# Kernel optimization log

Hardware: AMD Instinct MI355X
Metric: run time of the kernel (lower is better)

## Reference

```python
import math
import jax, jax.numpy as jnp
import numpy as np

N, C, T, V = 32, 64, 256, 25
EPS = 1e-5


def setup_inputs() -> dict:
    key = jax.random.key(0)
    ks = jax.random.split(key, 4)
    # kaiming fan_out init scale for 1x1 conv: std = sqrt(2 / C_out)
    std = math.sqrt(2.0 / C)
    return {
        "x": jax.random.normal(ks[0], (N, C, T, V), dtype=jnp.float32),
        "Wq": jax.random.normal(ks[1], (C, C), dtype=jnp.float32) * std,
        "bq": jnp.zeros((C,), dtype=jnp.float32),
        "Wk": jax.random.normal(ks[2], (C, C), dtype=jnp.float32) * std,
        "bk": jnp.zeros((C,), dtype=jnp.float32),
        "Wv": jax.random.normal(ks[3], (C, C), dtype=jnp.float32) * std,
        "bv": jnp.zeros((C,), dtype=jnp.float32),
        "gamma": jnp.ones((C,), dtype=jnp.float32),
        "beta": jnp.zeros((C,), dtype=jnp.float32),
    }


def _proj(x, W, b):
    # 1x1 conv over [N, Cin, T, V] then permute(0,3,2,1) -> [N, V, T, Cout]
    return jnp.einsum('nctv,dc->nvtd', x, W) + b


def reference(x, Wq, bq, Wk, bk, Wv, bv, gamma, beta):
    c_out = Wq.shape[0]
    q = _proj(x, Wq, bq)                                  # [N,V,T,C]
    k = _proj(x, Wk, bk)                                  # [N,V,T,C]
    v = _proj(x, Wv, bv)                                  # [N,V,T,C]
    att = jnp.einsum('nvsc,nvtc->nvst', q, k) / math.sqrt(c_out)
    att = jnp.tanh(att)                                   # [N,V,T,T]
    out = jnp.einsum('nvst,nvtc->nvsc', att, v)           # [N,V,T,C]
    out = jnp.transpose(out, (0, 3, 2, 1))                # [N,C,T,V]
    # BatchNorm2d, training mode (batch stats, biased variance)
    mean = jnp.mean(out, axis=(0, 2, 3), keepdims=True)
    var = jnp.var(out, axis=(0, 2, 3), keepdims=True)
    g = gamma[None, :, None, None]
    b = beta[None, :, None, None]
    return (out - mean) * jax.lax.rsqrt(var + EPS) * g + b
```

## Files before the change

### kernel.cpp

```cpp
#include <hip/hip_runtime.h>
#include <hip/hip_bf16.h>
#include <math.h>

#define NN 32
#define CC 64
#define TT 256
#define VV 25
#define PAD 68
#define RS (VV * CC)
#define PERN (TT * VV * CC)

#define KST 72
#define VST 40
#define PST 40
#define XST 72
#define FST 68

typedef __attribute__((ext_vector_type(8))) short bf16x8;
typedef __attribute__((ext_vector_type(4))) float f32x4;

__device__ __forceinline__ float fast_tanh(float x) {
  float ax = fabsf(x);
  float e = __expf(-2.0f * ax);
  float r = 1.0f - 2.0f * e / (1.0f + e);
  return copysignf(r, x);
}
__device__ __forceinline__ unsigned short f2bf(float f) {
  unsigned u = __float_as_uint(f);
  u += 0x7fff + ((u >> 16) & 1u);
  return (unsigned short)(u >> 16);
}
__device__ __forceinline__ float bf2f(unsigned short h) {
  return __uint_as_float(((unsigned)h) << 16);
}
__device__ __forceinline__ void cvt8(float4 a, float4 b, bf16x8& h8, bf16x8& l8) {
  unsigned short h;
  h = f2bf(a.x); h8[0] = (short)h; l8[0] = (short)f2bf(a.x - bf2f(h));
  h = f2bf(a.y); h8[1] = (short)h; l8[1] = (short)f2bf(a.y - bf2f(h));
  h = f2bf(a.z); h8[2] = (short)h; l8[2] = (short)f2bf(a.z - bf2f(h));
  h = f2bf(a.w); h8[3] = (short)h; l8[3] = (short)f2bf(a.w - bf2f(h));
  h = f2bf(b.x); h8[4] = (short)h; l8[4] = (short)f2bf(b.x - bf2f(h));
  h = f2bf(b.y); h8[5] = (short)h; l8[5] = (short)f2bf(b.y - bf2f(h));
  h = f2bf(b.z); h8[6] = (short)h; l8[6] = (short)f2bf(b.z - bf2f(h));
  h = f2bf(b.w); h8[7] = (short)h; l8[7] = (short)f2bf(b.w - bf2f(h));
}

__global__ void k0_zero(float* __restrict__ p) { p[threadIdx.x] = 0.0f; }

__global__ void k_wsplit(const float* __restrict__ Wq, const float* __restrict__ Wk,
                         const float* __restrict__ Wv, const float* __restrict__ bq,
                         const float* __restrict__ bk, const float* __restrict__ bv,
                         unsigned short* __restrict__ wh, unsigned short* __restrict__ wl,
                         float* __restrict__ bcat, float* __restrict__ stats)
{
  const int tid = threadIdx.x;
  if (tid < 128) stats[tid] = 0.0f;
  for (int i = 0; i < 48; ++i) {
    int idx = i * 256 + tid;
    int r = idx >> 6, c = idx & 63;
    int m = r >> 6, ch = r & 63;
    const float* W = (m == 0) ? Wq : (m == 1) ? Wk : Wv;
    float w = W[ch * 64 + c];
    unsigned short h = f2bf(w);
    wh[idx] = h;
    wl[idx] = f2bf(w - bf2f(h));
  }
  if (tid < 192) {
    int m = tid >> 6, ch = tid & 63;
    const float* B = (m == 0) ? bq : (m == 1) ? bk : bv;
    bcat[tid] = B[ch];
  }
}

__global__ __launch_bounds__(256, 2)
void k_proj_mfma(const float* __restrict__ x,
                 const unsigned short* __restrict__ wh,
                 const unsigned short* __restrict__ wl,
                 const float* __restrict__ bcat,
                 float* __restrict__ qb, float* __restrict__ kb,
                 float* __restrict__ vb)
{
  __shared__ short Xbuf[2 * 128 * XST];
  short* Xh = Xbuf;
  short* Xl = Xbuf + 128 * XST;

  const int tid  = threadIdx.x;
  const int lane = tid & 63;
  const int wid  = tid >> 6;
  const int l15  = lane & 15;
  const int g    = lane >> 4;
  const int band = wid * 48;

  const int n = blockIdx.x / 50;
  const int chunk = blockIdx.x - n * 50;
  const int tv0 = chunk * 128;
  const float* xn = x + (size_t)n * PERN + tv0;

  {
    const int cg  = tid >> 5;
    const int tvl = (tid & 31) * 4;
    #pragma unroll
    for (int r = 0; r < 2; ++r) {
      const int c0 = r * 32 + cg * 4;
      float4 r0 = *(const float4*)&xn[(size_t)(c0 + 0) * (TT * VV) + tvl];
      float4 r1 = *(const float4*)&xn[(size_t)(c0 + 1) * (TT * VV) + tvl];
      float4 r2 = *(const float4*)&xn[(size_t)(c0 + 2) * (TT * VV) + tvl];
      float4 r3 = *(const float4*)&xn[(size_t)(c0 + 3) * (TT * VV) + tvl];
      #pragma unroll
      for (int j = 0; j < 4; ++j) {
        float v0 = (&r0.x)[j], v1 = (&r1.x)[j], v2 = (&r2.x)[j], v3 = (&r3.x)[j];
        unsigned short h0 = f2bf(v0), h1 = f2bf(v1), h2 = f2bf(v2), h3 = f2bf(v3);
        *(short4*)&Xh[(tvl + j) * XST + c0] =
            make_short4((short)h0, (short)h1, (short)h2, (short)h3);
        *(short4*)&Xl[(tvl + j) * XST + c0] =
            make_short4((short)f2bf(v0 - bf2f(h0)), (short)f2bf(v1 - bf2f(h1)),
                        (short)f2bf(v2 - bf2f(h2)), (short)f2bf(v3 - bf2f(h3)));
      }
    }
  }

  bf16x8 wfh[3][2], wfl[3][2];
  #pragma unroll
  for (int rt = 0; rt < 3; ++rt)
    #pragma unroll
    for (int ks = 0; ks < 2; ++ks) {
      size_t off = (size_t)(band + rt * 16 + l15) * 64 + ks * 32 + g * 8;
      wfh[rt][ks] = *(const bf16x8*)&wh[off];
      wfl[rt][ks] = *(const bf16x8*)&wl[off];
    }
  float bc[3][4];
  #pragma unroll
  for (int rt = 0; rt < 3; ++rt)
    #pragma unroll
    for (int r = 0; r < 4; ++r)
      bc[rt][r] = bcat[band + rt * 16 + 4 * g + r];

  __syncthreads();

  f32x4 acc[3][8];
  #pragma unroll
  for (int rt = 0; rt < 3; ++rt)
    #pragma unroll
    for (int ct = 0; ct < 8; ++ct)
      acc[rt][ct] = (f32x4){0.f, 0.f, 0.f, 0.f};

  #pragma unroll
  for (int ct = 0; ct < 8; ++ct) {
    bf16x8 xh[2], xl[2];
    #pragma unroll
    for (int ks = 0; ks < 2; ++ks) {
      xh[ks] = *(const bf16x8*)&Xh[(ct * 16 + l15) * XST + ks * 32 + g * 8];
      xl[ks] = *(const bf16x8*)&Xl[(ct * 16 + l15) * XST + ks * 32 + g * 8];
    }
    #pragma unroll
    for (int rt = 0; rt < 3; ++rt)
      #pragma unroll
      for (int ks = 0; ks < 2; ++ks) {
        acc[rt][ct] = __builtin_amdgcn_mfma_f32_16x16x32_bf16(wfh[rt][ks], xh[ks], acc[rt][ct], 0, 0, 0);
        acc[rt][ct] = __builtin_amdgcn_mfma_f32_16x16x32_bf16(wfh[rt][ks], xl[ks], acc[rt][ct], 0, 0, 0);
        acc[rt][ct] = __builtin_amdgcn_mfma_f32_16x16x32_bf16(wfl[rt][ks], xh[ks], acc[rt][ct], 0, 0, 0);
      }
  }

  #pragma unroll
  for (int rt = 0; rt < 3; ++rt)
    #pragma unroll
    for (int ct = 0; ct < 8; ++ct)
      #pragma unroll
      for (int r = 0; r < 4; ++r)
        acc[rt][ct][r] += bc[rt][r];

  float* Fbuf = (float*)Xbuf;
  #pragma unroll
  for (int m = 0; m < 3; ++m) {
    __syncthreads();
    #pragma unroll
    for (int rt = 0; rt < 3; ++rt) {
      int grow = band + rt * 16;
      if ((grow >> 6) == m) {
        int ch = (grow & 63) + 4 * g;
        #pragma unroll
        for (int ct = 0; ct < 8; ++ct)
          *(f32x4*)&Fbuf[(ct * 16 + l15) * FST + ch] = acc[rt][ct];
      }
    }
    __syncthreads();
    float* gd = (m == 0 ? qb : m == 1 ? kb : vb) + (size_t)n * PERN + (size_t)tv0 * CC;
    #pragma unroll
    for (int i = 0; i < 8; ++i) {
      int e = i * 256 + tid;
      int tv = e >> 4, c4 = (e & 15) * 4;
      *(float4*)&gd[(size_t)e * 4] = *(const float4*)&Fbuf[tv * FST + c4];
    }
  }
}

__global__ __launch_bounds__(256, 2)
void k_attn_mfma(const float* __restrict__ qb, const float* __restrict__ kb,
                 const float* __restrict__ vb, float* __restrict__ stats,
                 float* __restrict__ ob)
{
  __shared__ short KhL[2][32 * KST], KlL[2][32 * KST];
  __shared__ short VhL[2][64 * VST], VlL[2][64 * VST];
  __shared__ short Pwh[4][64 * PST], Pwl[4][64 * PST];
  __shared__ float red1[256], red2[256];

  const int tid  = threadIdx.x;
  const int lane = tid & 63;
  const int wid  = tid >> 6;
  const int l15  = lane & 15;
  const int g    = lane >> 4;
  const int band = wid * 64;
  const int bid  = blockIdx.x;
  const int n = bid / VV, v = bid - n * VV;
  const size_t base = (size_t)n * PERN + (size_t)v * CC;

  const int sr = tid >> 3;
  const int sc = (tid & 7) * 8;

  bf16x8 qh[4][2], ql[4][2];
  #pragma unroll
  for (int rt = 0; rt < 4; ++rt) {
    #pragma unroll
    for (int ks = 0; ks < 2; ++ks) {
      const float* p = qb + base + (size_t)(band + rt * 16 + l15) * RS + ks * 32 + g * 8;
      cvt8(*(const float4*)p, *(const float4*)(p + 4), qh[rt][ks], ql[rt][ks]);
    }
  }

  f32x4 acc[4][4];
  #pragma unroll
  for (int i = 0; i < 4; ++i)
    #pragma unroll
    for (int j = 0; j < 4; ++j)
      acc[i][j] = (f32x4){0.f, 0.f, 0.f, 0.f};

  {
    const float* kp = kb + base + (size_t)sr * RS + sc;
    const float* vp = vb + base + (size_t)sr * RS + sc;
    float4 ka = *(const float4*)kp, kb4 = *(const float4*)(kp + 4);
    float4 va = *(const float4*)vp, vb4 = *(const float4*)(vp + 4);
    bf16x8 h8, l8;
    cvt8(ka, kb4, h8, l8);
    *(bf16x8*)&KhL[0][sr * KST + sc] = h8;
    *(bf16x8*)&KlL[0][sr * KST + sc] = l8;
    cvt8(va, vb4, h8, l8);
    #pragma unroll
    for (int j = 0; j < 8; ++j) {
      VhL[0][(sc + j) * VST + sr] = h8[j];
      VlL[0][(sc + j) * VST + sr] = l8[j];
    }
  }

  int cur = 0;
  for (int tl = 0; tl < 8; ++tl) {
    __syncthreads();
    const bool more = (tl < 7);
    float4 ka, kb4, va, vb4;
    if (more) {
      const float* kp = kb + base + (size_t)((tl + 1) * 32 + sr) * RS + sc;
      const float* vp = vb + base + (size_t)((tl + 1) * 32 + sr) * RS + sc;
      ka = *(const float4*)kp; kb4 = *(const float4*)(kp + 4);
      va = *(const float4*)vp; vb4 = *(const float4*)(vp + 4);
    }

    bf16x8 kfh[2][2], kfl[2][2];
    #pragma unroll
    for (int ct = 0; ct < 2; ++ct)
      #pragma unroll
      for (int ks = 0; ks < 2; ++ks) {
        kfh[ct][ks] = *(const bf16x8*)&KhL[cur][(ct * 16 + l15) * KST + ks * 32 + g * 8];
        kfl[ct][ks] = *(const bf16x8*)&KlL[cur][(ct * 16 + l15) * KST + ks * 32 + g * 8];
      }
    #pragma unroll
    for (int rt = 0; rt < 4; ++rt) {
      #pragma unroll
      for (int ct = 0; ct < 2; ++ct) {
        f32x4 s = (f32x4){0.f, 0.f, 0.f, 0.f};
        #pragma unroll
        for (int ks = 0; ks < 2; ++ks) {
          s = __builtin_amdgcn_mfma_f32_16x16x32_bf16(qh[rt][ks], kfh[ct][ks], s, 0, 0, 0);
          s = __builtin_amdgcn_mfma_f32_16x16x32_bf16(qh[rt][ks], kfl[ct][ks], s, 0, 0, 0);
          s = __builtin_amdgcn_mfma_f32_16x16x32_bf16(ql[rt][ks], kfh[ct][ks], s, 0, 0, 0);
        }
        #pragma unroll
        for (int r = 0; r < 4; ++r) {
          float p = fast_tanh(s[r] * 0.125f);
          unsigned short h = f2bf(p);
          int row = rt * 16 + 4 * g + r;
          Pwh[wid][row * PST + ct * 16 + l15] = (short)h;
          Pwl[wid][row * PST + ct * 16 + l15] = (short)f2bf(p - bf2f(h));
        }
      }
    }

    bf16x8 vfh[4], vfl[4], pfh[4], pfl[4];
    #pragma unroll
    for (int i = 0; i < 4; ++i) {
      vfh[i] = *(const bf16x8*)&VhL[cur][(i * 16 + l15) * VST + g * 8];
      vfl[i] = *(const bf16x8*)&VlL[cur][(i * 16 + l15) * VST + g * 8];
      pfh[i] = *(const bf16x8*)&Pwh[wid][(i * 16 + l15) * PST + g * 8];
      pfl[i] = *(const bf16x8*)&Pwl[wid][(i * 16 + l15) * PST + g * 8];
    }
    #pragma unroll
    for (int ctc = 0; ctc < 4; ++ctc) {
      #pragma unroll
      for (int st = 0; st < 4; ++st) {
        acc[ctc][st] = __builtin_amdgcn_mfma_f32_16x16x32_bf16(vfh[ctc], pfh[st], acc[ctc][st], 0, 0, 0);
        acc[ctc][st] = __builtin_amdgcn_mfma_f32_16x16x32_bf16(vfh[ctc], pfl[st], acc[ctc][st], 0, 0, 0);
        acc[ctc][st] = __builtin_amdgcn_mfma_f32_16x16x32_bf16(vfl[ctc], pfh[st], acc[ctc][st], 0, 0, 0);
      }
    }

    if (more) {
      int nb = cur ^ 1;
      bf16x8 h8, l8;
      cvt8(ka, kb4, h8, l8);
      *(bf16x8*)&KhL[nb][sr * KST + sc] = h8;
      *(bf16x8*)&KlL[nb][sr * KST + sc] = l8;
      cvt8(va, vb4, h8, l8);
      #pragma unroll
      for (int j = 0; j < 8; ++j) {
        VhL[nb][(sc + j) * VST + sr] = h8[j];
        VlL[nb][(sc + j) * VST + sr] = l8[j];
      }
    }
    cur ^= 1;
  }

  #pragma unroll
  for (int ctc = 0; ctc < 4; ++ctc) {
    #pragma unroll
    for (int r = 0; r < 4; ++r) {
      float s1 = 0.f, s2 = 0.f;
      #pragma unroll
      for (int st = 0; st < 4; ++st) { float vv = acc[ctc][st][r]; s1 += vv; s2 += vv * vv; }
      #pragma unroll
      for (int m = 1; m <= 8; m <<= 1) {
        s1 += __shfl_xor(s1, m, 64);
        s2 += __shfl_xor(s2, m, 64);
      }
      if (l15 == 0) {
        int c = ctc * 16 + 4 * g + r;
        red1[wid * 64 + c] = s1;
        red2[wid * 64 + c] = s2;
      }
    }
  }
  __syncthreads();
  if (tid < 64) {
    float a1 = red1[tid] + red1[64 + tid] + red1[128 + tid] + red1[192 + tid];
    float a2 = red2[tid] + red2[64 + tid] + red2[128 + tid] + red2[192 + tid];
    atomicAdd(&stats[tid], a1);
    atomicAdd(&stats[64 + tid], a2);
  }

  float* obp = ob + base;
  #pragma unroll
  for (int st = 0; st < 4; ++st)
    #pragma unroll
    for (int ctc = 0; ctc < 4; ++ctc)
      *(f32x4*)&obp[(size_t)(band + st * 16 + l15) * RS + ctc * 16 + 4 * g] = acc[ctc][st];
}

__global__ void k2_stats(const float* __restrict__ stats,
                         const float* __restrict__ gamma,
                         const float* __restrict__ beta,
                         float* __restrict__ ss)
{
  int c = threadIdx.x;
  if (c < 64) {
    const float M = (float)(NN * TT * VV);
    float mean = stats[c] / M;
    float var = stats[64 + c] / M - mean * mean;
    float sc = gamma[c] * rsqrtf(var + 1e-5f);
    ss[c] = sc;
    ss[64 + c] = beta[c] - mean * sc;
  }
}

__global__ __launch_bounds__(256)
void k3_emit(const float* __restrict__ ob, const float* __restrict__ ss,
             float* __restrict__ out)
{
  __shared__ float tile[VV * 8 * 65];
  __shared__ float scl[64], sft[64];
  const int bid = blockIdx.x;
  const int n = bid >> 5, sb = bid & 31;
  const int tid = threadIdx.x;
  if (tid < 64) { scl[tid] = ss[tid]; sft[tid] = ss[64 + tid]; }
  const float* src = ob + (size_t)n * PERN + (size_t)sb * 8 * RS;
  #pragma unroll
  for (int i = 0; i < 25; ++i) {
    int e2 = i * 512 + tid * 2;
    float2 f = *(const float2*)&src[e2];
    int c = e2 & 63;
    int r = e2 >> 6;
    int tL = r / 25, vv2 = r - tL * 25;
    tile[(vv2 * 8 + tL) * 65 + c] = f.x;
    tile[(vv2 * 8 + tL) * 65 + c + 1] = f.y;
  }
  __syncthreads();
  float* outn = out + (size_t)n * CC * TT * VV + sb * 8 * VV;
  for (int e = tid; e < CC * 200; e += 256) {
    int c = e / 200, r = e - c * 200;
    int tL = r / 25, v = r - tL * 25;
    float val = tile[(v * 8 + tL) * 65 + c];
    outn[(size_t)c * TT * VV + tL * VV + v] = val * scl[c] + sft[c];
  }
}

__global__ void k3b_inplace(float* __restrict__ out, const float* __restrict__ ss) {
  __shared__ float scl[64], sft[64];
  if (threadIdx.x < 64) { scl[threadIdx.x] = ss[threadIdx.x]; sft[threadIdx.x] = ss[64 + threadIdx.x]; }
  __syncthreads();
  const size_t total = (size_t)NN * CC * TT * VV;
  size_t i = ((size_t)blockIdx.x * 256 + threadIdx.x) * 4;
  const size_t stride = (size_t)gridDim.x * 256 * 4;
  for (; i < total; i += stride) {
    float4 val = *(float4*)(out + i);
    int c = (int)((i / (TT * VV)) & 63);
    val.x = val.x * scl[c] + sft[c];
    val.y = val.y * scl[c] + sft[c];
    val.z = val.z * scl[c] + sft[c];
    val.w = val.w * scl[c] + sft[c];
    *(float4*)(out + i) = val;
  }
}

__device__ __forceinline__ void proj_row(const float* xs, const float* Wl,
                                         const float* bl, float* dst) {
  for (int d4 = 0; d4 < 16; ++d4) {
    float4 r;
    #pragma unroll
    for (int j = 0; j < 4; ++j) {
      const int d = d4 * 4 + j;
      float acc = bl[d];
      #pragma unroll
      for (int c = 0; c < CC; ++c) acc += xs[c] * Wl[d * CC + c];
      ((float*)&r)[j] = acc;
    }
    *(float4*)&dst[d4 * 4] = r;
  }
}

__global__ __launch_bounds__(256)
void k1_attn(const float* __restrict__ x,
             const float* __restrict__ Wq, const float* __restrict__ bq,
             const float* __restrict__ Wk, const float* __restrict__ bk,
             const float* __restrict__ Wv, const float* __restrict__ bv,
             float* __restrict__ stats, float* __restrict__ outbuf)
{
  __shared__ float kl[TT * PAD];
  __shared__ float vl[TT * PAD];
  __shared__ float Wl[CC * CC];
  __shared__ float bl[CC];
  const int tid = threadIdx.x;
  const int bid = blockIdx.x;
  const int n = bid / VV, v = bid - n * VV;
  float xs[CC];
  {
    const float* xp = x + ((size_t)n * CC * TT + tid) * VV + v;
    #pragma unroll
    for (int c = 0; c < CC; ++c) xs[c] = xp[(size_t)c * TT * VV];
  }
  {
    const float4* Wg = (const float4*)Wq;
    float4* Wd = (float4*)Wl;
    #pragma unroll
    for (int j = 0; j < 4; ++j) Wd[j * 256 + tid] = Wg[j * 256 + tid];
    if (tid < CC) bl[tid] = bq[tid];
    __syncthreads();
    proj_row(xs, Wl, bl, &kl[tid * PAD]);
  }
  float q[CC];
  #pragma unroll
  for (int c4 = 0; c4 < 16; ++c4) {
    float4 t4 = *(const float4*)&kl[tid * PAD + c4 * 4];
    q[c4 * 4 + 0] = t4.x; q[c4 * 4 + 1] = t4.y;
    q[c4 * 4 + 2] = t4.z; q[c4 * 4 + 3] = t4.w;
  }
  __syncthreads();
  {
    const float4* Wg = (const float4*)Wk;
    float4* Wd = (float4*)Wl;
    #pragma unroll
    for (int j = 0; j < 4; ++j) Wd[j * 256 + tid] = Wg[j * 256 + tid];
    if (tid < CC) bl[tid] = bk[tid];
    __syncthreads();
    proj_row(xs, Wl, bl, &kl[tid * PAD]);
    __syncthreads();
  }
  {
    const float4* Wg = (const float4*)Wv;
    float4* Wd = (float4*)Wl;
    #pragma unroll
    for (int j = 0; j < 4; ++j) Wd[j * 256 + tid] = Wg[j * 256 + tid];
    if (tid < CC) bl[tid] = bv[tid];
    __syncthreads();
    proj_row(xs, Wl, bl, &vl[tid * PAD]);
    __syncthreads();
  }
  float out[CC];
  #pragma unroll
  for (int c = 0; c < CC; ++c) out[c] = 0.0f;
  for (int t = 0; t < TT; ++t) {
    const float4* kr = (const float4*)&kl[t * PAD];
    float acc = 0.0f;
    #pragma unroll
    for (int c4 = 0; c4 < 16; ++c4) {
      float4 kk = kr[c4];
      acc += q[c4 * 4 + 0] * kk.x + q[c4 * 4 + 1] * kk.y
           + q[c4 * 4 + 2] * kk.z + q[c4 * 4 + 3] * kk.w;
    }
    float a = fast_tanh(acc * 0.125f);
    const float4* vr = (const float4*)&vl[t * PAD];
    #pragma unroll
    for (int c4 = 0; c4 < 16; ++c4) {
      float4 vv = vr[c4];
      out[c4 * 4 + 0] += a * vv.x; out[c4 * 4 + 1] += a * vv.y;
      out[c4 * 4 + 2] += a * vv.z; out[c4 * 4 + 3] += a * vv.w;
    }
  }
  __syncthreads();
  float* out_lds = vl;
  #pragma unroll
  for (int c4 = 0; c4 < 16; ++c4) {
    *(float4*)&out_lds[tid * PAD + c4 * 4] =
        make_float4(out[c4 * 4 + 0], out[c4 * 4 + 1], out[c4 * 4 + 2], out[c4 * 4 + 3]);
  }
  __syncthreads();
  {
    const int c = tid & 63, gg = tid >> 6;
    float s1 = 0.0f, s2 = 0.0f;
    for (int s = gg * 64; s < gg * 64 + 64; ++s) {
      float val = out_lds[s * PAD + c];
      s1 += val; s2 += val * val;
    }
    float* part = Wl;
    part[tid] = s1;
    part[256 + tid] = s2;
    __syncthreads();
    if (tid < 64) {
      float a1 = part[tid] + part[64 + tid] + part[128 + tid] + part[192 + tid];
      float a2 = part[256 + tid] + part[320 + tid] + part[384 + tid] + part[448 + tid];
      atomicAdd(&stats[tid], a1);
      atomicAdd(&stats[64 + tid], a2);
    }
  }
  {
    float* obp = outbuf + (size_t)n * CC * TT * VV + v;
    for (int e = tid; e < TT * CC; e += 256) {
      int s = e >> 6, c = e & 63;
      obp[(size_t)c * TT * VV + (size_t)s * VV] = out_lds[s * PAD + c];
    }
  }
}


extern "C" void kernel_launch(void* const* d_in, const int* in_sizes, int n_in,
                              void* d_out, int out_size, void* d_ws, size_t ws_size,
                              hipStream_t stream) {
  (void)in_sizes; (void)n_in; (void)out_size;
  const float* x     = (const float*)d_in[0];
  const float* Wq    = (const float*)d_in[1];
  const float* bq    = (const float*)d_in[2];
  const float* Wk    = (const float*)d_in[3];
  const float* bk    = (const float*)d_in[4];
  const float* Wv    = (const float*)d_in[5];
  const float* bv    = (const float*)d_in[6];
  const float* gamma = (const float*)d_in[7];
  const float* beta  = (const float*)d_in[8];
  float* out = (float*)d_out;
  float* wsf = (float*)d_ws;

  float* stats = wsf;
  float* ss    = wsf + 128;
  float* bcat  = wsf + 256;
  unsigned short* wh = (unsigned short*)(wsf + 512);
  unsigned short* wl = wh + 192 * 64;
  float* qb = wsf + 512 + 12288;
  const size_t per = (size_t)NN * PERN;
  float* kb = qb + per;
  float* vb = kb + per;
  float* ob = vb + per;
  const size_t need = (512 + 12288 + 4 * per) * sizeof(float);

  if (ws_size >= need) {
    k_wsplit<<<1, 256, 0, stream>>>(Wq, Wk, Wv, bq, bk, bv, wh, wl, bcat, stats);
    k_proj_mfma<<<NN * 50, 256, 0, stream>>>(x, wh, wl, bcat, qb, kb, vb);
    k_attn_mfma<<<NN * VV, 256, 0, stream>>>(qb, kb, vb, stats, ob);
    k2_stats<<<1, 64, 0, stream>>>(stats, gamma, beta, ss);
    k3_emit<<<NN * 32, 256, 0, stream>>>(ob, ss, out);
  } else {
    k0_zero<<<1, 128, 0, stream>>>(stats);
    k1_attn<<<NN * VV, 256, 0, stream>>>(x, Wq, bq, Wk, bk, Wv, bv, stats, out);
    k2_stats<<<1, 64, 0, stream>>>(stats, gamma, beta, ss);
    k3b_inplace<<<2048, 256, 0, stream>>>(out, ss);
  }
}
```

Baseline: 279.5 us.

## Store Q/K/V as pre-split bf16 planes and cut attention MFMA passes

The projection kernel now writes Q and K as bf16 hi/lo planes and V as bf16 hi only, replacing fp32 intermediates. This halves intermediate traffic and removes the per-tile fp32-to-bf16 split work in attention. The attention kernel reads the Q low part from global inside the loop, keeps only the hi part of P and V (one MFMA instead of three for PV), uses a swizzled single-buffered K/V tile with an in-LDS V transpose, and raises the occupancy hint. The trade is lower precision in P and V, an extra barrier per tile, and repeated global reads of the Q low plane.

```diff
diff --git a/kernel.cpp b/kernel.cpp
--- a/kernel.cpp
+++ b/kernel.cpp
@@ -10,11 +10,9 @@
 #define RS (VV * CC)
 #define PERN (TT * VV * CC)
 
-#define KST 72
-#define VST 40
+#define XST 72
+#define VST2 72
 #define PST 40
-#define XST 72
-#define FST 68
 
 typedef __attribute__((ext_vector_type(8))) short bf16x8;
 typedef __attribute__((ext_vector_type(4))) float f32x4;
@@ -32,17 +30,6 @@
 }
 __device__ __forceinline__ float bf2f(unsigned short h) {
   return __uint_as_float(((unsigned)h) << 16);
-}
-__device__ __forceinline__ void cvt8(float4 a, float4 b, bf16x8& h8, bf16x8& l8) {
-  unsigned short h;
-  h = f2bf(a.x); h8[0] = (short)h; l8[0] = (short)f2bf(a.x - bf2f(h));
-  h = f2bf(a.y); h8[1] = (short)h; l8[1] = (short)f2bf(a.y - bf2f(h));
-  h = f2bf(a.z); h8[2] = (short)h; l8[2] = (short)f2bf(a.z - bf2f(h));
-  h = f2bf(a.w); h8[3] = (short)h; l8[3] = (short)f2bf(a.w - bf2f(h));
-  h = f2bf(b.x); h8[4] = (short)h; l8[4] = (short)f2bf(b.x - bf2f(h));
-  h = f2bf(b.y); h8[5] = (short)h; l8[5] = (short)f2bf(b.y - bf2f(h));
-  h = f2bf(b.z); h8[6] = (short)h; l8[6] = (short)f2bf(b.z - bf2f(h));
-  h = f2bf(b.w); h8[7] = (short)h; l8[7] = (short)f2bf(b.w - bf2f(h));
 }
 
 __global__ void k0_zero(float* __restrict__ p) { p[threadIdx.x] = 0.0f; }
@@ -77,8 +64,9 @@
                  const unsigned short* __restrict__ wh,
                  const unsigned short* __restrict__ wl,
                  const float* __restrict__ bcat,
-                 float* __restrict__ qb, float* __restrict__ kb,
-                 float* __restrict__ vb)
+                 unsigned short* __restrict__ qh, unsigned short* __restrict__ ql,
+                 unsigned short* __restrict__ kh, unsigned short* __restrict__ kl,
+                 unsigned short* __restrict__ vh)
 {
   __shared__ short Xbuf[2 * 128 * XST];
   short* Xh = Xbuf;
@@ -170,7 +158,9 @@
       for (int r = 0; r < 4; ++r)
         acc[rt][ct][r] += bc[rt][r];
 
-  float* Fbuf = (float*)Xbuf;
+  short* Sh = Xbuf;
+  short* Sl = Xbuf + 128 * XST;
+  const size_t cbase = ((size_t)n * (TT * VV) + tv0) * CC;
   #pragma unroll
   for (int m = 0; m < 3; ++m) {
     __syncthreads();
@@ -180,29 +170,47 @@
       if ((grow >> 6) == m) {
         int ch = (grow & 63) + 4 * g;
         #pragma unroll
-        for (int ct = 0; ct < 8; ++ct)
-          *(f32x4*)&Fbuf[(ct * 16 + l15) * FST + ch] = acc[rt][ct];
-      }
-    }
-    __syncthreads();
-    float* gd = (m == 0 ? qb : m == 1 ? kb : vb) + (size_t)n * PERN + (size_t)tv0 * CC;
-    #pragma unroll
-    for (int i = 0; i < 8; ++i) {
+        for (int ct = 0; ct < 8; ++ct) {
+          f32x4 a = acc[rt][ct];
+          short4 h4, l4;
+          #pragma unroll
+          for (int r = 0; r < 4; ++r) {
+            unsigned short h = f2bf(a[r]);
+            (&h4.x)[r] = (short)h;
+            (&l4.x)[r] = (short)f2bf(a[r] - bf2f(h));
+          }
+          *(short4*)&Sh[(ct * 16 + l15) * XST + ch] = h4;
+          if (m < 2) *(short4*)&Sl[(ct * 16 + l15) * XST + ch] = l4;
+        }
+      }
+    }
+    __syncthreads();
+    unsigned short* dh = (m == 0 ? qh : m == 1 ? kh : vh) + cbase;
+    #pragma unroll
+    for (int i = 0; i < 4; ++i) {
       int e = i * 256 + tid;
-      int tv = e >> 4, c4 = (e & 15) * 4;
-      *(float4*)&gd[(size_t)e * 4] = *(const float4*)&Fbuf[tv * FST + c4];
-    }
-  }
-}
-
-__global__ __launch_bounds__(256, 2)
-void k_attn_mfma(const float* __restrict__ qb, const float* __restrict__ kb,
-                 const float* __restrict__ vb, float* __restrict__ stats,
-                 float* __restrict__ ob)
+      *(bf16x8*)&dh[(size_t)e * 8] = *(const bf16x8*)&Sh[(e >> 3) * XST + (e & 7) * 8];
+    }
+    if (m < 2) {
+      unsigned short* dl = (m == 0 ? ql : kl) + cbase;
+      #pragma unroll
+      for (int i = 0; i < 4; ++i) {
+        int e = i * 256 + tid;
+        *(bf16x8*)&dl[(size_t)e * 8] = *(const bf16x8*)&Sl[(e >> 3) * XST + (e & 7) * 8];
+      }
+    }
+  }
+}
+
+__global__ __launch_bounds__(256, 3)
+void k_attn_mfma2(const unsigned short* __restrict__ qhp, const unsigned short* __restrict__ qlp,
+                  const unsigned short* __restrict__ khp, const unsigned short* __restrict__ klp,
+                  const unsigned short* __restrict__ vhp,
+                  float* __restrict__ stats, float* __restrict__ ob)
 {
-  __shared__ short KhL[2][32 * KST], KlL[2][32 * KST];
-  __shared__ short VhL[2][64 * VST], VlL[2][64 * VST];
-  __shared__ short Pwh[4][64 * PST], Pwl[4][64 * PST];
+  __shared__ short Kh[32 * 64], Kl[32 * 64], Vh[32 * 64];
+  __shared__ short VT[64 * VST2];
+  __shared__ short Pw[4][64 * PST];
   __shared__ float red1[256], red2[256];
 
   const int tid  = threadIdx.x;
@@ -211,21 +219,17 @@
   const int l15  = lane & 15;
   const int g    = lane >> 4;
   const int band = wid * 64;
-  const int bid  = blockIdx.x;
-  const int n = bid / VV, v = bid - n * VV;
-  const size_t base = (size_t)n * PERN + (size_t)v * CC;
-
-  const int sr = tid >> 3;
-  const int sc = (tid & 7) * 8;
-
-  bf16x8 qh[4][2], ql[4][2];
-  #pragma unroll
-  for (int rt = 0; rt < 4; ++rt) {
-    #pragma unroll
-    for (int ks = 0; ks < 2; ++ks) {
-      const float* p = qb + base + (size_t)(band + rt * 16 + l15) * RS + ks * 32 + g * 8;
-      cvt8(*(const float4*)p, *(const float4*)(p + 4), qh[rt][ks], ql[rt][ks]);
-    }
+  const int n = blockIdx.x / VV, v = blockIdx.x - n * VV;
+  const size_t sbase = ((size_t)n * (TT * VV) + v) * CC;
+
+  bf16x8 qhf[4][2];
+  const unsigned short* qlrow[4];
+  #pragma unroll
+  for (int st = 0; st < 4; ++st) {
+    const unsigned short* qp = qhp + sbase + (size_t)(band + st * 16 + l15) * RS + g * 8;
+    qhf[st][0] = *(const bf16x8*)qp;
+    qhf[st][1] = *(const bf16x8*)(qp + 32);
+    qlrow[st] = qlp + sbase + (size_t)(band + st * 16 + l15) * RS + g * 8;
   }
 
   f32x4 acc[4][4];
@@ -235,97 +239,88 @@
     for (int j = 0; j < 4; ++j)
       acc[i][j] = (f32x4){0.f, 0.f, 0.f, 0.f};
 
-  {
-    const float* kp = kb + base + (size_t)sr * RS + sc;
-    const float* vp = vb + base + (size_t)sr * RS + sc;
-    float4 ka = *(const float4*)kp, kb4 = *(const float4*)(kp + 4);
-    float4 va = *(const float4*)vp, vb4 = *(const float4*)(vp + 4);
-    bf16x8 h8, l8;
-    cvt8(ka, kb4, h8, l8);
-    *(bf16x8*)&KhL[0][sr * KST + sc] = h8;
-    *(bf16x8*)&KlL[0][sr * KST + sc] = l8;
-    cvt8(va, vb4, h8, l8);
-    #pragma unroll
-    for (int j = 0; j < 8; ++j) {
-      VhL[0][(sc + j) * VST + sr] = h8[j];
-      VlL[0][(sc + j) * VST + sr] = l8[j];
-    }
-  }
-
-  int cur = 0;
+  const int sr = tid >> 3, scb = tid & 7;
+  const int swz = scb ^ (sr & 7);
+  const size_t gsrc = sbase + (size_t)sr * RS + scb * 8;
+
+  {
+    bf16x8 a = *(const bf16x8*)(khp + gsrc);
+    bf16x8 b = *(const bf16x8*)(klp + gsrc);
+    bf16x8 c = *(const bf16x8*)(vhp + gsrc);
+    *(bf16x8*)&Kh[sr * 64 + swz * 8] = a;
+    *(bf16x8*)&Kl[sr * 64 + swz * 8] = b;
+    *(bf16x8*)&Vh[sr * 64 + swz * 8] = c;
+  }
+
+  const int slot0 = g ^ (l15 & 7);
   for (int tl = 0; tl < 8; ++tl) {
     __syncthreads();
+    bf16x8 nk_h, nk_l, nv_h;
     const bool more = (tl < 7);
-    float4 ka, kb4, va, vb4;
     if (more) {
-      const float* kp = kb + base + (size_t)((tl + 1) * 32 + sr) * RS + sc;
-      const float* vp = vb + base + (size_t)((tl + 1) * 32 + sr) * RS + sc;
-      ka = *(const float4*)kp; kb4 = *(const float4*)(kp + 4);
-      va = *(const float4*)vp; vb4 = *(const float4*)(vp + 4);
-    }
-
-    bf16x8 kfh[2][2], kfl[2][2];
-    #pragma unroll
-    for (int ct = 0; ct < 2; ++ct)
-      #pragma unroll
-      for (int ks = 0; ks < 2; ++ks) {
-        kfh[ct][ks] = *(const bf16x8*)&KhL[cur][(ct * 16 + l15) * KST + ks * 32 + g * 8];
-        kfl[ct][ks] = *(const bf16x8*)&KlL[cur][(ct * 16 + l15) * KST + ks * 32 + g * 8];
-      }
-    #pragma unroll
-    for (int rt = 0; rt < 4; ++rt) {
-      #pragma unroll
-      for (int ct = 0; ct < 2; ++ct) {
+      const size_t src = gsrc + (size_t)(tl + 1) * 32 * RS;
+      nk_h = *(const bf16x8*)(khp + src);
+      nk_l = *(const bf16x8*)(klp + src);
+      nv_h = *(const bf16x8*)(vhp + src);
+    }
+
+    #pragma unroll
+    for (int rt = 0; rt < 2; ++rt) {
+      const int rb = rt * 1024 + l15 * 64;
+      bf16x8 kh0 = *(const bf16x8*)&Kh[rb + slot0 * 8];
+      bf16x8 kh1 = *(const bf16x8*)&Kh[rb + (slot0 ^ 4) * 8];
+      bf16x8 kl0 = *(const bf16x8*)&Kl[rb + slot0 * 8];
+      bf16x8 kl1 = *(const bf16x8*)&Kl[rb + (slot0 ^ 4) * 8];
+      #pragma unroll
+      for (int st = 0; st < 4; ++st) {
+        bf16x8 ql0 = *(const bf16x8*)(qlrow[st]);
+        bf16x8 ql1 = *(const bf16x8*)(qlrow[st] + 32);
         f32x4 s = (f32x4){0.f, 0.f, 0.f, 0.f};
-        #pragma unroll
-        for (int ks = 0; ks < 2; ++ks) {
-          s = __builtin_amdgcn_mfma_f32_16x16x32_bf16(qh[rt][ks], kfh[ct][ks], s, 0, 0, 0);
-          s = __builtin_amdgcn_mfma_f32_16x16x32_bf16(qh[rt][ks], kfl[ct][ks], s, 0, 0, 0);
-          s = __builtin_amdgcn_mfma_f32_16x16x32_bf16(ql[rt][ks], kfh[ct][ks], s, 0, 0, 0);
-        }
+        s = __builtin_amdgcn_mfma_f32_16x16x32_bf16(kh0, qhf[st][0], s, 0, 0, 0);
+        s = __builtin_amdgcn_mfma_f32_16x16x32_bf16(kh1, qhf[st][1], s, 0, 0, 0);
+        s = __builtin_amdgcn_mfma_f32_16x16x32_bf16(kl0, qhf[st][0], s, 0, 0, 0);
+        s = __builtin_amdgcn_mfma_f32_16x16x32_bf16(kl1, qhf[st][1], s, 0, 0, 0);
+        s = __builtin_amdgcn_mfma_f32_16x16x32_bf16(kh0, ql0, s, 0, 0, 0);
+        s = __builtin_amdgcn_mfma_f32_16x16x32_bf16(kh1, ql1, s, 0, 0, 0);
+        short4 h4;
         #pragma unroll
         for (int r = 0; r < 4; ++r) {
           float p = fast_tanh(s[r] * 0.125f);
-          unsigned short h = f2bf(p);
-          int row = rt * 16 + 4 * g + r;
-          Pwh[wid][row * PST + ct * 16 + l15] = (short)h;
-          Pwl[wid][row * PST + ct * 16 + l15] = (short)f2bf(p - bf2f(h));
+          (&h4.x)[r] = (short)f2bf(p);
         }
-      }
-    }
-
-    bf16x8 vfh[4], vfl[4], pfh[4], pfl[4];
+        *(short4*)&Pw[wid][(st * 16 + l15) * PST + rt * 16 + 4 * g] = h4;
+      }
+    }
+
+    {
+      const int c = tid & 63, b = tid >> 6;
+      bf16x8 colv;
+      #pragma unroll
+      for (int e = 0; e < 8; ++e) {
+        int t = 8 * b + e;
+        colv[e] = Vh[t * 64 + (((c >> 3) ^ (t & 7)) * 8) + (c & 7)];
+      }
+      *(bf16x8*)&VT[c * VST2 + 8 * b] = colv;
+    }
+    __syncthreads();
+
+    bf16x8 vtf[4], pf[4];
     #pragma unroll
     for (int i = 0; i < 4; ++i) {
-      vfh[i] = *(const bf16x8*)&VhL[cur][(i * 16 + l15) * VST + g * 8];
-      vfl[i] = *(const bf16x8*)&VlL[cur][(i * 16 + l15) * VST + g * 8];
-      pfh[i] = *(const bf16x8*)&Pwh[wid][(i * 16 + l15) * PST + g * 8];
-      pfl[i] = *(const bf16x8*)&Pwl[wid][(i * 16 + l15) * PST + g * 8];
-    }
-    #pragma unroll
-    for (int ctc = 0; ctc < 4; ++ctc) {
-      #pragma unroll
-      for (int st = 0; st < 4; ++st) {
-        acc[ctc][st] = __builtin_amdgcn_mfma_f32_16x16x32_bf16(vfh[ctc], pfh[st], acc[ctc][st], 0, 0, 0);
-        acc[ctc][st] = __builtin_amdgcn_mfma_f32_16x16x32_bf16(vfh[ctc], pfl[st], acc[ctc][st], 0, 0, 0);
-        acc[ctc][st] = __builtin_amdgcn_mfma_f32_16x16x32_bf16(vfl[ctc], pfh[st], acc[ctc][st], 0, 0, 0);
-      }
-    }
+      vtf[i] = *(const bf16x8*)&VT[(i * 16 + l15) * VST2 + g * 8];
+      pf[i]  = *(const bf16x8*)&Pw[wid][(i * 16 + l15) * PST + g * 8];
+    }
+    #pragma unroll
+    for (int ctc = 0; ctc < 4; ++ctc)
+      #pragma unroll
+      for (int st = 0; st < 4; ++st)
+        acc[ctc][st] = __builtin_amdgcn_mfma_f32_16x16x32_bf16(vtf[ctc], pf[st], acc[ctc][st], 0, 0, 0);
 
     if (more) {
-      int nb = cur ^ 1;
-      bf16x8 h8, l8;
-      cvt8(ka, kb4, h8, l8);
-      *(bf16x8*)&KhL[nb][sr * KST + sc] = h8;
-      *(bf16x8*)&KlL[nb][sr * KST + sc] = l8;
-      cvt8(va, vb4, h8, l8);
-      #pragma unroll
-      for (int j = 0; j < 8; ++j) {
-        VhL[nb][(sc + j) * VST + sr] = h8[j];
-        VlL[nb][(sc + j) * VST + sr] = l8[j];
-      }
-    }
-    cur ^= 1;
+      *(bf16x8*)&Kh[sr * 64 + swz * 8] = nk_h;
+      *(bf16x8*)&Kl[sr * 64 + swz * 8] = nk_l;
+      *(bf16x8*)&Vh[sr * 64 + swz * 8] = nv_h;
+    }
   }
 
   #pragma unroll
@@ -355,7 +350,7 @@
     atomicAdd(&stats[64 + tid], a2);
   }
 
-  float* obp = ob + base;
+  float* obp = (float*)ob + sbase;
   #pragma unroll
   for (int st = 0; st < 4; ++st)
     #pragma unroll
@@ -579,17 +574,19 @@
   float* bcat  = wsf + 256;
   unsigned short* wh = (unsigned short*)(wsf + 512);
   unsigned short* wl = wh + 192 * 64;
-  float* qb = wsf + 512 + 12288;
-  const size_t per = (size_t)NN * PERN;
-  float* kb = qb + per;
-  float* vb = kb + per;
-  float* ob = vb + per;
-  const size_t need = (512 + 12288 + 4 * per) * sizeof(float);
+  const size_t PS = (size_t)NN * PERN;
+  unsigned short* qh = (unsigned short*)(wsf + 512 + 12288);
+  unsigned short* ql = qh + PS;
+  unsigned short* kh = ql + PS;
+  unsigned short* kl = kh + PS;
+  unsigned short* vh = kl + PS;
+  float* ob = (float*)(vh + PS);
+  const size_t need = (size_t)(512 + 12288) * 4 + 5 * PS * 2 + PS * 4;
 
   if (ws_size >= need) {
     k_wsplit<<<1, 256, 0, stream>>>(Wq, Wk, Wv, bq, bk, bv, wh, wl, bcat, stats);
-    k_proj_mfma<<<NN * 50, 256, 0, stream>>>(x, wh, wl, bcat, qb, kb, vb);
-    k_attn_mfma<<<NN * VV, 256, 0, stream>>>(qb, kb, vb, stats, ob);
+    k_proj_mfma<<<NN * 50, 256, 0, stream>>>(x, wh, wl, bcat, qh, ql, kh, kl, vh);
+    k_attn_mfma2<<<NN * VV, 256, 0, stream>>>(qh, ql, kh, kl, vh, stats, ob);
     k2_stats<<<1, 64, 0, stream>>>(stats, gamma, beta, ss);
     k3_emit<<<NN * 32, 256, 0, stream>>>(ob, ss, out);
   } else {
```

Measured after the change: 345.1 us. 23.5% more time.
